# Optimization experiments

Measured on AMD Instinct MI355X. Metric: run time of the kernel, lower is better.

The kernel has to match this reference:

```python
import jax, jax.numpy as jnp
import numpy as np

BN_EPS = 1e-5


def _xavier(key, fan_in, fan_out):
    lim = np.sqrt(6.0 / (fan_in + fan_out))
    return jax.random.uniform(key, (fan_in, fan_out), jnp.float32, -lim, lim)


def setup_inputs() -> dict:
    key = jax.random.key(0)
    ks = jax.random.split(key, 4)
    B = 262144
    x = jax.random.normal(ks[0], (B, 15), jnp.float32)
    # fixed lookup-table buffers from __init__
    temp_set = jnp.array([18.0, 20, 22, 24, 26, 28, 30, 31.5, 32], jnp.float32)
    temp_envr = jnp.array([-30.0, -20, -10, 0, 5, 10, 15, 20, 25, 30, 35, 40, 45, 50], jnp.float32)
    cabin_table = jnp.array([
        [17.0, 17, 17, 17, 17, 17, 17, 17, 17, 17, 17, 17, 17, 17],
        [20, 20, 19.5, 19.5, 19.5, 19, 19, 19, 18.5, 18.5, 18, 18, 18, 18],
        [22, 22, 22, 22.5, 22.5, 22.5, 22, 22, 21, 21, 21, 21, 20.5, 20],
        [24, 24.5, 25.5, 25.5, 26, 26, 25.5, 25, 24.5, 24, 23.5, 23, 23, 23],
        [27, 26.5, 27, 27.5, 28, 28, 27.5, 27, 26.5, 26, 25.5, 26, 26, 26],
        [29, 28.5, 28.5, 29.5, 30, 30, 29.5, 29, 29, 29, 28, 28, 29, 29],
        [31, 30.5, 30.5, 31.5, 32, 32, 32, 31, 31, 31, 31, 31, 31, 31],
        [32, 32, 32, 33, 33, 33, 33, 33, 33, 33, 33, 33, 32, 32],
        [32, 32, 36, 36, 36, 36, 36, 36, 36, 36, 36, 36, 36, 36]], jnp.float32)
    # MLP 4 -> 512 -> 512 -> 1, xavier-uniform weights, zero bias
    w1 = _xavier(ks[1], 4, 512)
    w2 = _xavier(ks[2], 512, 512)
    w3 = _xavier(ks[3], 512, 1)
    z = jnp.zeros
    return {
        'x': x, 'temp_set': temp_set, 'temp_envr': temp_envr, 'cabin_table': cabin_table,
        'w1': w1, 'b1': z((512,)), 'g1': jnp.ones((512,)), 'beta1': z((512,)),
        'w2': w2, 'b2': z((512,)), 'g2': jnp.ones((512,)), 'beta2': z((512,)),
        'w3': w3, 'b3': z((1,)),
    }


def inter2d(xs, ys, table, xq, yq):
    """Bilinear interpolation on table[len(xs), len(ys)] at (xq, yq), clamped to range."""
    xq = jnp.clip(xq, xs[0], xs[-1])
    yq = jnp.clip(yq, ys[0], ys[-1])
    i = jnp.clip(jnp.searchsorted(xs, xq, side='right') - 1, 0, xs.shape[0] - 2)
    j = jnp.clip(jnp.searchsorted(ys, yq, side='right') - 1, 0, ys.shape[0] - 2)
    x0, x1 = xs[i], xs[i + 1]
    y0, y1 = ys[j], ys[j + 1]
    tx = (xq - x0) / (x1 - x0)
    ty = (yq - y0) / (y1 - y0)
    f00 = table[i, j]
    f01 = table[i, j + 1]
    f10 = table[i + 1, j]
    f11 = table[i + 1, j + 1]
    return (f00 * (1 - tx) * (1 - ty) + f10 * tx * (1 - ty)
            + f01 * (1 - tx) * ty + f11 * tx * ty)


def _batchnorm_train(h, g, b):
    # BatchNorm1d in training mode: biased batch statistics
    mu = jnp.mean(h, axis=0)
    var = jnp.mean((h - mu) ** 2, axis=0)
    return g * (h - mu) * jax.lax.rsqrt(var + BN_EPS) + b


def reference(x, temp_set, temp_envr, cabin_table,
              w1, b1, g1, beta1, w2, b2, g2, beta2, w3, b3):
    temp_amb = x[:, 1]
    cab_fl_set_temp = x[:, 2]
    cab_fr_set_temp = x[:, 3]
    temp_incar = x[:, 8]
    temp_battery_req = x[:, 9]
    temp_coolant_battery_in = x[:, 10]

    dvt_fl = inter2d(temp_set, temp_envr, cabin_table, cab_fl_set_temp, temp_amb) - temp_incar
    dvt_fr = inter2d(temp_set, temp_envr, cabin_table, cab_fr_set_temp, temp_amb) - temp_incar
    dct = temp_battery_req - temp_coolant_battery_in

    use_x1 = jnp.stack([dvt_fl, dvt_fr, temp_amb, dct], axis=1)  # [B, 4]

    h = jnp.tanh(_batchnorm_train(use_x1 @ w1 + b1, g1, beta1))  # [B, 512]
    h = jnp.tanh(_batchnorm_train(h @ w2 + b2, g2, beta2))       # [B, 512]
    return h @ w3 + b3                                           # [B, 1]
```

## Files before the change

### kernel.cpp

```cpp
#include <hip/hip_runtime.h>

typedef unsigned int u32;
typedef unsigned short u16;
typedef __bf16 bf16x8 __attribute__((ext_vector_type(8)));
typedef float f32x16 __attribute__((ext_vector_type(16)));
typedef u32 u32x4 __attribute__((ext_vector_type(4)));
typedef _Float16 f16x2 __attribute__((ext_vector_type(2)));
typedef _Float16 f16x8 __attribute__((ext_vector_type(8)));

#define TANH_PRESCALE 2.8853900817779268f

__device__ __forceinline__ u16 f2bf(float f) {
  u32 u = __float_as_uint(f);
  u32 r = (u + 0x7FFFu + ((u >> 16) & 1u)) >> 16;
  return (u16)r;
}
__device__ __forceinline__ float bf2f(u16 h) {
  return __uint_as_float((u32)h << 16);
}
__device__ __forceinline__ u32 cvtpk_bf16(float a, float b) {
  u32 r;
  asm("v_cvt_pk_bf16_f32 %0, %1, %2" : "=v"(r) : "v"(a), "v"(b));
  return r;
}
__device__ __forceinline__ u32 packf16(float a, float b) {
  f16x2 h;
  h[0] = (_Float16)a;
  h[1] = (_Float16)b;
  return __builtin_bit_cast(u32, h);
}
__device__ __forceinline__ float tanh_pre(float v) {
  float e = __builtin_exp2f(v);
  return 1.0f - 2.0f * __builtin_amdgcn_rcpf(e + 1.0f);
}

__device__ __forceinline__ float inter2d_d(const float* xs, const float* ys,
                                           const float* tb, float xq, float yq) {
  xq = fminf(fmaxf(xq, xs[0]), xs[8]);
  yq = fminf(fmaxf(yq, ys[0]), ys[13]);
  int i = 0, j = 0;
#pragma unroll
  for (int k = 1; k <= 8; ++k) if (xq >= xs[k]) i = k;
#pragma unroll
  for (int k = 1; k <= 13; ++k) if (yq >= ys[k]) j = k;
  if (i > 7) i = 7;
  if (j > 12) j = 12;
  float x0 = xs[i], x1 = xs[i + 1], y0 = ys[j], y1 = ys[j + 1];
  float tx = (xq - x0) / (x1 - x0);
  float ty = (yq - y0) / (y1 - y0);
  float f00 = tb[i * 14 + j], f01 = tb[i * 14 + j + 1];
  float f10 = tb[(i + 1) * 14 + j], f11 = tb[(i + 1) * 14 + j + 1];
  return f00 * (1 - tx) * (1 - ty) + f10 * tx * (1 - ty) +
         f01 * (1 - tx) * ty + f11 * tx * ty;
}

__global__ void pre_kernel(const float* __restrict__ x,
                           const float* __restrict__ tsg,
                           const float* __restrict__ teg,
                           const float* __restrict__ tbg,
                           float* __restrict__ mom,
                           const float* __restrict__ w2,
                           unsigned char* __restrict__ w2ts, int nstat) {
  __shared__ float ts[9], te[14], tb[126], bacc[14];
  int t = threadIdx.x;
  if ((int)blockIdx.x >= nstat) {
    int q = ((int)blockIdx.x - nstat) * 256 + t;
    int n = q & 511;
    int kb = (q >> 9) * 8;
    u32 pk[4];
#pragma unroll
    for (int e = 0; e < 8; e += 2) {
      u16 a = f2bf(w2[(size_t)(kb + e) * 512 + n]);
      u16 b = f2bf(w2[(size_t)(kb + e + 1) * 512 + n]);
      pk[e >> 1] = (u32)a | ((u32)b << 16);
    }
    *(uint4*)(w2ts + (size_t)q * 16) = make_uint4(pk[0], pk[1], pk[2], pk[3]);
    return;
  }
  if (t < 9) ts[t] = tsg[t];
  if (t < 14) { te[t] = teg[t]; bacc[t] = 0.f; }
  if (t < 126) tb[t] = tbg[t];
  __syncthreads();
  const float* xr = x + (size_t)(blockIdx.x * 256 + t) * 15;
  float amb = xr[1], inc = xr[8];
  float u0 = inter2d_d(ts, te, tb, xr[2], amb) - inc;
  float u1 = inter2d_d(ts, te, tb, xr[3], amb) - inc;
  float u2 = amb, u3 = xr[9] - xr[10];
  float v[14] = {u0, u1, u2, u3,
                 u0 * u0, u0 * u1, u0 * u2, u0 * u3,
                 u1 * u1, u1 * u2, u1 * u3,
                 u2 * u2, u2 * u3, u3 * u3};
#pragma unroll
  for (int i = 0; i < 14; ++i) {
    float s = v[i];
    s += __shfl_xor(s, 32); s += __shfl_xor(s, 16); s += __shfl_xor(s, 8);
    s += __shfl_xor(s, 4);  s += __shfl_xor(s, 2);  s += __shfl_xor(s, 1);
    v[i] = s;
  }
  if ((t & 63) == 0)
    for (int i = 0; i < 14; ++i) atomicAdd(&bacc[i], v[i]);
  __syncthreads();
  if (t < 14) atomicAdd(&mom[t], bacc[t]);
}

__global__ void prep1_kernel(const float* __restrict__ mom,
                             const float* __restrict__ w1,
                             const float* __restrict__ g1,
                             const float* __restrict__ be1,
                             unsigned char* __restrict__ a1img, float invB) {
  int j = threadIdx.x;
  float m0 = mom[0] * invB, m1 = mom[1] * invB, m2 = mom[2] * invB, m3 = mom[3] * invB;
  float C00 = mom[4]  * invB - m0 * m0, C01 = mom[5]  * invB - m0 * m1;
  float C02 = mom[6]  * invB - m0 * m2, C03 = mom[7]  * invB - m0 * m3;
  float C11 = mom[8]  * invB - m1 * m1, C12 = mom[9]  * invB - m1 * m2;
  float C13 = mom[10] * invB - m1 * m3, C22 = mom[11] * invB - m2 * m2;
  float C23 = mom[12] * invB - m2 * m3, C33 = mom[13] * invB - m3 * m3;
  float a = w1[j], b = w1[512 + j], c = w1[1024 + j], d = w1[1536 + j];
  float var = a * a * C00 + b * b * C11 + c * c * C22 + d * d * C33 +
              2.f * (a * b * C01 + a * c * C02 + a * d * C03 +
                     b * c * C12 + b * d * C13 + c * d * C23);
  float s1 = g1[j] * rsqrtf(fmaxf(var, 0.f) + 1e-5f) * TANH_PRESCALE;
  float a0 = a * s1, a1 = b * s1, a2 = c * s1, a3 = d * s1;
  float c1j = be1[j] * TANH_PRESCALE -
              (m0 * a + m1 * b + m2 * c + m3 * d) * s1;
  u16 ba0 = f2bf(a0), ba1 = f2bf(a1), ba2 = f2bf(a2), ba3 = f2bf(a3);
  u16 da0 = f2bf(a0 - bf2f(ba0)), da1 = f2bf(a1 - bf2f(ba1));
  u16 da2 = f2bf(a2 - bf2f(ba2)), da3 = f2bf(a3 - bf2f(ba3));
  u16 c1h = f2bf(c1j);
  u16 c1l = f2bf(c1j - bf2f(c1h));
  u32 p01 = (u32)ba0 | ((u32)ba1 << 16);
  u32 p23 = (u32)ba2 | ((u32)ba3 << 16);
  uint4* img = (uint4*)a1img;
  img[j * 2]     = make_uint4(p01, p23, (u32)c1h | ((u32)da0 << 16),
                              (u32)da1 | ((u32)da2 << 16));
  img[j * 2 + 1] = make_uint4(p01, p23, (u32)c1l | ((u32)da3 << 16), 0u);
}

__global__ __launch_bounds__(1024) void gemm12_kernel(
    const float* __restrict__ x, const float* __restrict__ tsg,
    const float* __restrict__ teg, const float* __restrict__ tbg,
    const unsigned char* __restrict__ a1img,
    const unsigned char* __restrict__ w2ts, float* __restrict__ stat2,
    unsigned char* __restrict__ t2buf, int nstore) {
  __shared__ __align__(16) unsigned char sm_buf[2][32768];
  __shared__ __align__(16) float sm_u[128][4];
  __shared__ float sm_ts[9], sm_te[14], sm_tb[126];

  const int t = threadIdx.x;
  const int w = t >> 6, l = t & 63;
  const int hi = l >> 5, ln = l & 31;
  const int wm = w >> 3;
  const int wn = w & 7;
  const int rt = w & 3;
  const int jt = w >> 2;
  const int r0 = blockIdx.x * 128;

  if (t < 9) sm_ts[t] = tsg[t];
  if (t < 14) sm_te[t] = teg[t];
  if (t < 126) sm_tb[t] = tbg[t];
  __syncthreads();

  if (t < 128) {
    const float* xr = x + (size_t)(r0 + t) * 15;
    float amb = xr[1], inc = xr[8];
    sm_u[t][0] = inter2d_d(sm_ts, sm_te, sm_tb, xr[2], amb) - inc;
    sm_u[t][1] = inter2d_d(sm_ts, sm_te, sm_tb, xr[3], amb) - inc;
    sm_u[t][2] = amb;
    sm_u[t][3] = xr[9] - xr[10];
  }
  __syncthreads();

  bf16x8 ufrag;
  {
    float4 uv = *(const float4*)&sm_u[rt * 32 + ln][0];
    u16 b0_ = f2bf(uv.x), b1_ = f2bf(uv.y), b2_ = f2bf(uv.z), b3_ = f2bf(uv.w);
    u32x4 uq;
    if (hi == 0) {
      uq[0] = (u32)b0_ | ((u32)b1_ << 16);
      uq[1] = (u32)b2_ | ((u32)b3_ << 16);
      uq[2] = 0x00003F80u | ((u32)b0_ << 16);
      uq[3] = (u32)b1_ | ((u32)b2_ << 16);
    } else {
      u16 d0 = f2bf(uv.x - bf2f(b0_)), d1 = f2bf(uv.y - bf2f(b1_));
      u16 d2 = f2bf(uv.z - bf2f(b2_)), d3 = f2bf(uv.w - bf2f(b3_));
      uq[0] = (u32)d0 | ((u32)d1 << 16);
      uq[1] = (u32)d2 | ((u32)d3 << 16);
      uq[2] = 0x00003F80u | ((u32)b3_ << 16);
      uq[3] = 0u;
    }
    ufrag = __builtin_bit_cast(bf16x8, uq);
  }

  auto produce = [&](int sl) {
    unsigned char* dst = sm_buf[sl & 1];
    bf16x8 af = *(const bf16x8*)(a1img +
        ((size_t)(sl * 128 + jt * 32 + ln) * 32 + hi * 16));
    f32x16 z = {};
    f32x16 d = __builtin_amdgcn_mfma_f32_32x32x16_bf16(af, ufrag, z, 0, 0, 0);
#pragma unroll
    for (int q = 0; q < 4; ++q) {
      u32 plo = cvtpk_bf16(tanh_pre(d[q * 4 + 0]), tanh_pre(d[q * 4 + 1]));
      u32 phi = cvtpk_bf16(tanh_pre(d[q * 4 + 2]), tanh_pre(d[q * 4 + 3]));
      *(uint2*)(dst + ((size_t)((jt * 4 + q) * 128 + rt * 32 + ln) * 16 + hi * 8)) =
          make_uint2(plo, phi);
    }
  };

  auto loadB = [&](uint4* dst, int ks) {
    const unsigned char* p = w2ts + ((size_t)(ks * 2 + hi) * 8192) +
                             (size_t)(wn * 64 + ln) * 16;
    dst[0] = *(const uint4*)(p);
    dst[1] = *(const uint4*)(p + 512);
  };

  f32x16 acc[4];
#pragma unroll
  for (int i = 0; i < 4; ++i)
#pragma unroll
    for (int k = 0; k < 16; ++k) acc[i][k] = 0.0f;

  uint4 bb[2][2];
  loadB(bb[0], 0);
  produce(0);
  __syncthreads();

#pragma unroll
  for (int sl = 0; sl < 4; ++sl) {
    const unsigned char* abuf = sm_buf[sl & 1];
#pragma unroll
    for (int s = 0; s < 8; ++s) {
      int ks = sl * 8 + s;
      if (ks < 31) loadB(bb[(ks + 1) & 1], ks + 1);
      const unsigned char* ab =
          abuf + ((size_t)(2 * s + hi) * 128 + wm * 64 + ln) * 16;
      bf16x8 a0 = *(const bf16x8*)(ab);
      bf16x8 a1 = *(const bf16x8*)(ab + 512);
#pragma unroll
      for (int nf = 0; nf < 2; ++nf) {
        bf16x8 bv = __builtin_bit_cast(bf16x8, bb[ks & 1][nf]);
        acc[0 + nf] = __builtin_amdgcn_mfma_f32_32x32x16_bf16(a0, bv, acc[0 + nf], 0, 0, 0);
        acc[2 + nf] = __builtin_amdgcn_mfma_f32_32x32x16_bf16(a1, bv, acc[2 + nf], 0, 0, 0);
      }
      if (s == 0 && sl < 3) produce(sl + 1);
    }
    __syncthreads();
  }

  if (blockIdx.x < (u32)nstore) {
    uint4* dst = (uint4*)(t2buf + (size_t)blockIdx.x * 131072);
#pragma unroll
    for (int i = 0; i < 4; ++i)
#pragma unroll
      for (int h2 = 0; h2 < 2; ++h2) {
        uint4 pk4;
        pk4.x = packf16(acc[i][h2 * 8 + 0], acc[i][h2 * 8 + 1]);
        pk4.y = packf16(acc[i][h2 * 8 + 2], acc[i][h2 * 8 + 3]);
        pk4.z = packf16(acc[i][h2 * 8 + 4], acc[i][h2 * 8 + 5]);
        pk4.w = packf16(acc[i][h2 * 8 + 6], acc[i][h2 * 8 + 7]);
        dst[(i * 2 + h2) * 1024 + t] = pk4;
      }
  }
#pragma unroll
  for (int nf = 0; nf < 2; ++nf) {
    float s = 0.f, q = 0.f;
#pragma unroll
    for (int mf = 0; mf < 2; ++mf)
#pragma unroll
      for (int k = 0; k < 16; ++k) {
        float v = acc[mf * 2 + nf][k];
        s += v; q += v * v;
      }
    s += __shfl_xor(s, 32); q += __shfl_xor(q, 32);
    if (hi == 0) {
      int col = wn * 64 + nf * 32 + ln;
      atomicAdd(&stat2[col], s);
      atomicAdd(&stat2[512 + col], q);
    }
  }
}

__global__ __launch_bounds__(1024) void finish_kernel(
    const float* __restrict__ x, const float* __restrict__ tsg,
    const float* __restrict__ teg, const float* __restrict__ tbg,
    const unsigned char* __restrict__ a1img,
    const unsigned char* __restrict__ w2ts,
    const float* __restrict__ stat2,
    const unsigned char* __restrict__ t2buf,
    const float* __restrict__ g2, const float* __restrict__ be2,
    const float* __restrict__ w3g, const float* __restrict__ b3g,
    float* __restrict__ out, int nstore, float invB) {
  __shared__ __align__(16) unsigned char sm_buf[2][32768];
  __shared__ __align__(16) float sm_u[128][4];
  __shared__ float sm_ts[9], sm_te[14], sm_tb[126];

  const int t = threadIdx.x;
  const int w = t >> 6, l = t & 63;
  const int hi = l >> 5, ln = l & 31;
  const int wm = w >> 3;
  const int wn = w & 7;
  const int rt = w & 3;
  const int jt = w >> 2;
  const int r0 = blockIdx.x * 128;

  float sv[2], cv[2], wv[2];
#pragma unroll
  for (int nf = 0; nf < 2; ++nf) {
    int col = wn * 64 + nf * 32 + ln;
    float mu = stat2[col] * invB;
    float ex2 = stat2[512 + col] * invB;
    float var = fmaxf(ex2 - mu * mu, 0.f);
    float s = g2[col] * rsqrtf(var + 1e-5f);
    sv[nf] = s * TANH_PRESCALE;
    cv[nf] = (be2[col] - mu * s) * TANH_PRESCALE;
    wv[nf] = w3g[col];
  }
  float* pr = (float*)sm_buf[0];

  if (blockIdx.x < (u32)nstore) {
    const uint4* src = (const uint4*)(t2buf + (size_t)blockIdx.x * 131072);
#pragma unroll
    for (int mf = 0; mf < 2; ++mf) {
      uint4 q[2][2];
#pragma unroll
      for (int nf = 0; nf < 2; ++nf)
#pragma unroll
        for (int h2 = 0; h2 < 2; ++h2)
          q[nf][h2] = src[((mf * 2 + nf) * 2 + h2) * 1024 + t];
#pragma unroll
      for (int k = 0; k < 16; ++k) {
        float v = 0.f;
#pragma unroll
        for (int nf = 0; nf < 2; ++nf) {
          f16x8 qq = __builtin_bit_cast(f16x8, q[nf][k >> 3]);
          float a0 = (float)qq[k & 7];
          v += tanh_pre(a0 * sv[nf] + cv[nf]) * wv[nf];
        }
        v += __shfl_xor(v, 1); v += __shfl_xor(v, 2); v += __shfl_xor(v, 4);
        v += __shfl_xor(v, 8); v += __shfl_xor(v, 16);
        if (ln == 0) {
          int row = wm * 64 + mf * 32 + (k & 3) + 8 * (k >> 2) + 4 * hi;
          pr[row * 8 + wn] = v;
        }
      }
    }
    __syncthreads();
    if (t < 128) {
      float s = b3g[0];
#pragma unroll
      for (int i = 0; i < 8; ++i) s += pr[t * 8 + i];
      out[r0 + t] = s;
    }
    return;
  }

  if (t < 9) sm_ts[t] = tsg[t];
  if (t < 14) sm_te[t] = teg[t];
  if (t < 126) sm_tb[t] = tbg[t];
  __syncthreads();

  if (t < 128) {
    const float* xr = x + (size_t)(r0 + t) * 15;
    float amb = xr[1], inc = xr[8];
    sm_u[t][0] = inter2d_d(sm_ts, sm_te, sm_tb, xr[2], amb) - inc;
    sm_u[t][1] = inter2d_d(sm_ts, sm_te, sm_tb, xr[3], amb) - inc;
    sm_u[t][2] = amb;
    sm_u[t][3] = xr[9] - xr[10];
  }
  __syncthreads();

  bf16x8 ufrag;
  {
    float4 uv = *(const float4*)&sm_u[rt * 32 + ln][0];
    u16 b0_ = f2bf(uv.x), b1_ = f2bf(uv.y), b2_ = f2bf(uv.z), b3_ = f2bf(uv.w);
    u32x4 uq;
    if (hi == 0) {
      uq[0] = (u32)b0_ | ((u32)b1_ << 16);
      uq[1] = (u32)b2_ | ((u32)b3_ << 16);
      uq[2] = 0x00003F80u | ((u32)b0_ << 16);
      uq[3] = (u32)b1_ | ((u32)b2_ << 16);
    } else {
      u16 d0 = f2bf(uv.x - bf2f(b0_)), d1 = f2bf(uv.y - bf2f(b1_));
      u16 d2 = f2bf(uv.z - bf2f(b2_)), d3 = f2bf(uv.w - bf2f(b3_));
      uq[0] = (u32)d0 | ((u32)d1 << 16);
      uq[1] = (u32)d2 | ((u32)d3 << 16);
      uq[2] = 0x00003F80u | ((u32)b3_ << 16);
      uq[3] = 0u;
    }
    ufrag = __builtin_bit_cast(bf16x8, uq);
  }

  auto produce = [&](int sl) {
    unsigned char* dst = sm_buf[sl & 1];
    bf16x8 af = *(const bf16x8*)(a1img +
        ((size_t)(sl * 128 + jt * 32 + ln) * 32 + hi * 16));
    f32x16 z = {};
    f32x16 d = __builtin_amdgcn_mfma_f32_32x32x16_bf16(af, ufrag, z, 0, 0, 0);
#pragma unroll
    for (int q = 0; q < 4; ++q) {
      u32 plo = cvtpk_bf16(tanh_pre(d[q * 4 + 0]), tanh_pre(d[q * 4 + 1]));
      u32 phi = cvtpk_bf16(tanh_pre(d[q * 4 + 2]), tanh_pre(d[q * 4 + 3]));
      *(uint2*)(dst + ((size_t)((jt * 4 + q) * 128 + rt * 32 + ln) * 16 + hi * 8)) =
          make_uint2(plo, phi);
    }
  };

  auto loadB = [&](uint4* dst, int ks) {
    const unsigned char* p = w2ts + ((size_t)(ks * 2 + hi) * 8192) +
                             (size_t)(wn * 64 + ln) * 16;
    dst[0] = *(const uint4*)(p);
    dst[1] = *(const uint4*)(p + 512);
  };

  f32x16 acc[4];
#pragma unroll
  for (int i = 0; i < 4; ++i)
#pragma unroll
    for (int k = 0; k < 16; ++k) acc[i][k] = 0.0f;

  uint4 bb[2][2];
  loadB(bb[0], 0);
  produce(0);
  __syncthreads();

#pragma unroll
  for (int sl = 0; sl < 4; ++sl) {
    const unsigned char* abuf = sm_buf[sl & 1];
#pragma unroll
    for (int s = 0; s < 8; ++s) {
      int ks = sl * 8 + s;
      if (ks < 31) loadB(bb[(ks + 1) & 1], ks + 1);
      const unsigned char* ab =
          abuf + ((size_t)(2 * s + hi) * 128 + wm * 64 + ln) * 16;
      bf16x8 a0 = *(const bf16x8*)(ab);
      bf16x8 a1 = *(const bf16x8*)(ab + 512);
#pragma unroll
      for (int nf = 0; nf < 2; ++nf) {
        bf16x8 bv = __builtin_bit_cast(bf16x8, bb[ks & 1][nf]);
        acc[0 + nf] = __builtin_amdgcn_mfma_f32_32x32x16_bf16(a0, bv, acc[0 + nf], 0, 0, 0);
        acc[2 + nf] = __builtin_amdgcn_mfma_f32_32x32x16_bf16(a1, bv, acc[2 + nf], 0, 0, 0);
      }
      if (s == 0 && sl < 3) produce(sl + 1);
    }
    __syncthreads();
  }

#pragma unroll
  for (int mf = 0; mf < 2; ++mf)
#pragma unroll
    for (int k = 0; k < 16; ++k) {
      float v = tanh_pre(acc[mf * 2 + 0][k] * sv[0] + cv[0]) * wv[0] +
                tanh_pre(acc[mf * 2 + 1][k] * sv[1] + cv[1]) * wv[1];
      v += __shfl_xor(v, 1); v += __shfl_xor(v, 2); v += __shfl_xor(v, 4);
      v += __shfl_xor(v, 8); v += __shfl_xor(v, 16);
      if (ln == 0) {
        int row = wm * 64 + mf * 32 + (k & 3) + 8 * (k >> 2) + 4 * hi;
        pr[row * 8 + wn] = v;
      }
    }
  __syncthreads();
  if (t < 128) {
    float s = b3g[0];
#pragma unroll
    for (int i = 0; i < 8; ++i) s += pr[t * 8 + i];
    out[r0 + t] = s;
  }
}

extern "C" void kernel_launch(void* const* d_in, const int* in_sizes, int n_in,
                              void* d_out, int out_size, void* d_ws, size_t ws_size,
                              hipStream_t stream) {
  const float* x   = (const float*)d_in[0];
  const float* ts  = (const float*)d_in[1];
  const float* te  = (const float*)d_in[2];
  const float* tab = (const float*)d_in[3];
  const float* w1  = (const float*)d_in[4];
  const float* g1  = (const float*)d_in[6];
  const float* be1 = (const float*)d_in[7];
  const float* w2  = (const float*)d_in[8];
  const float* g2  = (const float*)d_in[10];
  const float* be2 = (const float*)d_in[11];
  const float* w3  = (const float*)d_in[12];
  const float* b3  = (const float*)d_in[13];
  float* out = (float*)d_out;
  char* ws = (char*)d_ws;

  if (ws_size < (size_t)(32768 + 524288)) return;

  int Bn = in_sizes[0] / 15;
  float invB = 1.0f / (float)Bn;
  int ntiles = Bn / 128;
  int nstat = Bn / 256;

  float* mom   = (float*)(ws + 0);
  float* stat2 = (float*)(ws + 64);
  unsigned char* a1img = (unsigned char*)(ws + 4160);
  unsigned char* w2ts = (unsigned char*)(ws + 32768);
  unsigned char* t2buf = (unsigned char*)(ws + (1 << 20));

  size_t avail = ws_size > (size_t)(1 << 20) ? ws_size - (size_t)(1 << 20) : 0;
  size_t cap = avail / 131072;
  int nstore = cap >= (size_t)ntiles ? ntiles : (int)cap;

  (void)hipMemsetAsync(ws, 0, 4160, stream);
  pre_kernel<<<nstat + 128, 256, 0, stream>>>(x, ts, te, tab, mom, w2, w2ts, nstat);
  prep1_kernel<<<1, 512, 0, stream>>>(mom, w1, g1, be1, a1img, invB);
  gemm12_kernel<<<ntiles, 1024, 0, stream>>>(x, ts, te, tab, a1img, w2ts,
                                             stat2, t2buf, nstore);
  finish_kernel<<<ntiles, 1024, 0, stream>>>(x, ts, te, tab, a1img, w2ts,
                                             stat2, t2buf, g2, be2, w3, b3,
                                             out, nstore, invB);
}
```

Before: 409.1 us.

## Store stashed layer-2 pre-activations row-major via LDS transpose, simplify finish reduction

```diff
diff --git a/kernel.cpp b/kernel.cpp
--- a/kernel.cpp
+++ b/kernel.cpp
@@ -23,11 +23,9 @@
   asm("v_cvt_pk_bf16_f32 %0, %1, %2" : "=v"(r) : "v"(a), "v"(b));
   return r;
 }
-__device__ __forceinline__ u32 packf16(float a, float b) {
-  f16x2 h;
-  h[0] = (_Float16)a;
-  h[1] = (_Float16)b;
-  return __builtin_bit_cast(u32, h);
+__device__ __forceinline__ u16 f2h_bits(float a) {
+  _Float16 h = (_Float16)a;
+  return __builtin_bit_cast(u16, h);
 }
 __device__ __forceinline__ float tanh_pre(float v) {
   float e = __builtin_exp2f(v);
@@ -142,7 +140,7 @@
     const unsigned char* __restrict__ a1img,
     const unsigned char* __restrict__ w2ts, float* __restrict__ stat2,
     unsigned char* __restrict__ t2buf, int nstore) {
-  __shared__ __align__(16) unsigned char sm_buf[2][32768];
+  __shared__ __align__(16) unsigned char sm_buf[2][33280];
   __shared__ __align__(16) float sm_u[128][4];
   __shared__ float sm_ts[9], sm_te[14], sm_tb[126];
 
@@ -247,19 +245,34 @@
   }
 
   if (blockIdx.x < (u32)nstore) {
-    uint4* dst = (uint4*)(t2buf + (size_t)blockIdx.x * 131072);
-#pragma unroll
-    for (int i = 0; i < 4; ++i)
-#pragma unroll
-      for (int h2 = 0; h2 < 2; ++h2) {
-        uint4 pk4;
-        pk4.x = packf16(acc[i][h2 * 8 + 0], acc[i][h2 * 8 + 1]);
-        pk4.y = packf16(acc[i][h2 * 8 + 2], acc[i][h2 * 8 + 3]);
-        pk4.z = packf16(acc[i][h2 * 8 + 4], acc[i][h2 * 8 + 5]);
-        pk4.w = packf16(acc[i][h2 * 8 + 6], acc[i][h2 * 8 + 7]);
-        dst[(i * 2 + h2) * 1024 + t] = pk4;
+    u16* lds16 = (u16*)sm_buf;
+#pragma unroll
+    for (int mf = 0; mf < 2; ++mf) {
+#pragma unroll
+      for (int nf = 0; nf < 2; ++nf) {
+        int col = wn * 64 + nf * 32 + ln;
+#pragma unroll
+        for (int k = 0; k < 16; ++k) {
+          int lr = wm * 32 + (k & 3) + 8 * (k >> 2) + 4 * hi;
+          lds16[lr * 520 + col] = f2h_bits(acc[mf * 2 + nf][k]);
+        }
       }
-  }
+      __syncthreads();
+      int lr = t >> 4;
+      int grow = (lr >> 5) * 64 + mf * 32 + (lr & 31);
+      uint4* gdst = (uint4*)(t2buf + (size_t)blockIdx.x * 131072 +
+                             (size_t)grow * 1024);
+      const uint4* lsrc =
+          (const uint4*)((const unsigned char*)lds16 + (size_t)lr * 1040);
+#pragma unroll
+      for (int c = 0; c < 4; ++c) {
+        int cb = (t & 15) + 16 * c;
+        gdst[cb] = lsrc[cb];
+      }
+      __syncthreads();
+    }
+  }
+
 #pragma unroll
   for (int nf = 0; nf < 2; ++nf) {
     float s = 0.f, q = 0.f;
@@ -289,7 +302,7 @@
     const float* __restrict__ g2, const float* __restrict__ be2,
     const float* __restrict__ w3g, const float* __restrict__ b3g,
     float* __restrict__ out, int nstore, float invB) {
-  __shared__ __align__(16) unsigned char sm_buf[2][32768];
+  __shared__ __align__(16) unsigned char sm_buf[2][33280];
   __shared__ __align__(16) float sm_u[128][4];
   __shared__ float sm_ts[9], sm_te[14], sm_tb[126];
 
@@ -301,6 +314,38 @@
   const int rt = w & 3;
   const int jt = w >> 2;
   const int r0 = blockIdx.x * 128;
+
+  if (blockIdx.x < (u32)nstore) {
+    float sv8[8], cv8[8], wv8[8];
+    int cbase = l * 8;
+#pragma unroll
+    for (int j = 0; j < 8; ++j) {
+      int col = cbase + j;
+      float mu = stat2[col] * invB;
+      float ex2 = stat2[512 + col] * invB;
+      float var = fmaxf(ex2 - mu * mu, 0.f);
+      float s = g2[col] * rsqrtf(var + 1e-5f);
+      sv8[j] = s * TANH_PRESCALE;
+      cv8[j] = (be2[col] - mu * s) * TANH_PRESCALE;
+      wv8[j] = w3g[col];
+    }
+    const unsigned char* tile = t2buf + (size_t)blockIdx.x * 131072;
+    float b3v = b3g[0];
+#pragma unroll
+    for (int rr = 0; rr < 8; ++rr) {
+      int r = w * 8 + rr;
+      uint4 q = *(const uint4*)(tile + (size_t)r * 1024 + (size_t)l * 16);
+      f16x8 qq = __builtin_bit_cast(f16x8, q);
+      float v = 0.f;
+#pragma unroll
+      for (int j = 0; j < 8; ++j)
+        v += tanh_pre((float)qq[j] * sv8[j] + cv8[j]) * wv8[j];
+      v += __shfl_xor(v, 1); v += __shfl_xor(v, 2); v += __shfl_xor(v, 4);
+      v += __shfl_xor(v, 8); v += __shfl_xor(v, 16); v += __shfl_xor(v, 32);
+      if (l == 0) out[r0 + r] = b3v + v;
+    }
+    return;
+  }
 
   float sv[2], cv[2], wv[2];
 #pragma unroll
@@ -315,43 +360,6 @@
     wv[nf] = w3g[col];
   }
   float* pr = (float*)sm_buf[0];
-
-  if (blockIdx.x < (u32)nstore) {
-    const uint4* src = (const uint4*)(t2buf + (size_t)blockIdx.x * 131072);
-#pragma unroll
-    for (int mf = 0; mf < 2; ++mf) {
-      uint4 q[2][2];
-#pragma unroll
-      for (int nf = 0; nf < 2; ++nf)
-#pragma unroll
-        for (int h2 = 0; h2 < 2; ++h2)
-          q[nf][h2] = src[((mf * 2 + nf) * 2 + h2) * 1024 + t];
-#pragma unroll
-      for (int k = 0; k < 16; ++k) {
-        float v = 0.f;
-#pragma unroll
-        for (int nf = 0; nf < 2; ++nf) {
-          f16x8 qq = __builtin_bit_cast(f16x8, q[nf][k >> 3]);
-          float a0 = (float)qq[k & 7];
-          v += tanh_pre(a0 * sv[nf] + cv[nf]) * wv[nf];
-        }
-        v += __shfl_xor(v, 1); v += __shfl_xor(v, 2); v += __shfl_xor(v, 4);
-        v += __shfl_xor(v, 8); v += __shfl_xor(v, 16);
-        if (ln == 0) {
-          int row = wm * 64 + mf * 32 + (k & 3) + 8 * (k >> 2) + 4 * hi;
-          pr[row * 8 + wn] = v;
-        }
-      }
-    }
-    __syncthreads();
-    if (t < 128) {
-      float s = b3g[0];
-#pragma unroll
-      for (int i = 0; i < 8; ++i) s += pr[t * 8 + i];
-      out[r0 + t] = s;
-    }
-    return;
-  }
 
   if (t < 9) sm_ts[t] = tsg[t];
   if (t < 14) sm_te[t] = teg[t];
```

Measured after the change: 418.8 us. +2.4%, slower.
